# Optimization experiments

Hardware: AMD Instinct MI355X
Metric: run time of the kernel (lower is better)

Reference implementation:

```python
import jax, jax.numpy as jnp
import numpy as np

N, H, G = 500_000, 128, 50_000


def setup_inputs() -> dict:
    key = jax.random.key(0)
    k1, k2, k3, k4, k5, k6, k7 = jax.random.split(key, 7)
    x_src = jax.random.normal(k1, (N, H), dtype=jnp.float32)
    imputed_embs = jax.random.normal(k2, (G, H), dtype=jnp.float32)
    src_ids = jnp.sort(jax.random.randint(k3, (N,), 0, G, dtype=jnp.int32))
    s = 1.0 / np.sqrt(2 * H)
    W1 = jax.random.uniform(k4, (H, 2 * H), jnp.float32, -s, s)  # cat_linear1
    b1 = jax.random.uniform(k5, (H,), jnp.float32, -s, s)
    W2 = jax.random.uniform(k6, (H, 2 * H), jnp.float32, -s, s)  # cat_linear2
    b2 = jax.random.uniform(k7, (H,), jnp.float32, -s, s)
    return {"x_src": x_src, "imputed_embs": imputed_embs, "W1": W1, "b1": b1,
            "W2": W2, "b2": b2, "src_ids": src_ids}


def reference(x_src, imputed_embs, W1, b1, W2, b2, src_ids):
    n, h = x_src.shape
    g = imputed_embs.shape[0]
    # group index per row: boundaries where adjacent sorted src_ids differ
    boundary = jnp.concatenate([jnp.zeros((1,), jnp.int32),
                                (src_ids[1:] != src_ids[:-1]).astype(jnp.int32)])
    gid = jnp.cumsum(boundary)  # [N] group id (0..num_groups-1)
    # segment mean of x_src per group (parallel replacement of the python loop)
    seg_sum = jax.ops.segment_sum(x_src, gid, num_segments=g)
    counts = jax.ops.segment_sum(jnp.ones((n,), x_src.dtype), gid, num_segments=g)
    seg_mean = seg_sum / jnp.maximum(counts, 1.0)[:, None]
    # original loop never writes the mean for the LAST group (or unused rows):
    written = (jnp.arange(g) < gid[-1])[:, None]
    imp_second = jnp.where(written, seg_mean, imputed_embs)
    # x_out rows: [x_src_i, imputed_embs[group(i)]]
    x_cat = jnp.concatenate([x_src, imputed_embs[gid]], axis=1)      # [N, 2H]
    imp_cat = jnp.concatenate([imputed_embs, imp_second], axis=1)    # [G, 2H]
    x_out = x_cat @ W1.T + b1
    imputed_out = imp_cat @ W2.T + b2
    return (x_out, imputed_out)
```

## Files before the change

kernel.cpp:

```cpp
#include <hip/hip_runtime.h>

typedef __attribute__((ext_vector_type(8))) short short8;
typedef __attribute__((ext_vector_type(4))) float f32x4;

static __device__ __forceinline__ unsigned short f2bf(float f) {
    union { float f; unsigned int u; } v; v.f = f;
    unsigned int r = v.u + 0x7fffu + ((v.u >> 16) & 1u);
    return (unsigned short)(r >> 16);
}

static __device__ __forceinline__ short8 pack8(float4 a, float4 b) {
    short8 r;
    r[0] = (short)f2bf(a.x); r[1] = (short)f2bf(a.y);
    r[2] = (short)f2bf(a.z); r[3] = (short)f2bf(a.w);
    r[4] = (short)f2bf(b.x); r[5] = (short)f2bf(b.y);
    r[6] = (short)f2bf(b.z); r[7] = (short)f2bf(b.w);
    return r;
}

static __device__ __forceinline__ void dma16(const void* g, void* l) {
    __builtin_amdgcn_global_load_lds(
        (const __attribute__((address_space(1))) unsigned int*)g,
        (__attribute__((address_space(3))) unsigned int*)l, 16, 0, 0);
}

static __device__ __forceinline__ float4 lds_rd16(const float* buf, int boff, int sw) {
    return *(const float4*)((const char*)buf + (boff ^ sw));
}

__global__ void k_zero(uint4* p, int n16) {
    int i = blockIdx.x * blockDim.x + threadIdx.x;
    if (i < n16) p[i] = uint4{0u, 0u, 0u, 0u};
}

__global__ void k_convw(const float* __restrict__ W1, const float* __restrict__ W2,
                        unsigned short* W1af, unsigned short* W1bf,
                        unsigned short* W2af, unsigned short* W2bf) {
    int T = blockIdx.x * 256 + threadIdx.x;
    int mat = T >> 11;
    int rem = T & 2047;
    int f = rem >> 6, lane = rem & 63;
    int wc = f >> 4, t = (f >> 2) & 3, kk = f & 3;
    int p = lane & 15, q = lane >> 4;
    int row = wc * 64 + t * 16 + p;
    int col = (mat & 1) * 128 + kk * 32 + q * 8;
    const float* src = (mat < 2 ? W1 : W2) + row * 256 + col;
    unsigned short* dst = (mat == 0 ? W1af : mat == 1 ? W1bf : mat == 2 ? W2af : W2bf);
    short8 v;
#pragma unroll
    for (int j = 0; j < 8; ++j) v[j] = (short)f2bf(src[j]);
    *(short8*)&dst[(size_t)f * 512 + lane * 8] = v;
}

__global__ void k_mark(const int* __restrict__ ids, int* __restrict__ cum, int n) {
    int i = blockIdx.x * blockDim.x + threadIdx.x;
    if (i < n) cum[ids[i]] = 1;
}

__global__ __launch_bounds__(256) void k_scan1(int* __restrict__ cum, int* __restrict__ bsum, int G) {
    __shared__ int ws[4];
    int tid = threadIdx.x;
    int base = blockIdx.x * 1024 + tid * 4;
    int a0 = 0, a1 = 0, a2 = 0, a3 = 0;
    if (base + 0 < G) a0 = cum[base + 0];
    if (base + 1 < G) a1 = cum[base + 1];
    if (base + 2 < G) a2 = cum[base + 2];
    if (base + 3 < G) a3 = cum[base + 3];
    int s = a0 + a1 + a2 + a3;
    int lane = tid & 63;
    int v = s;
#pragma unroll
    for (int off = 1; off < 64; off <<= 1) {
        int u = __shfl_up(v, off, 64);
        if (lane >= off) v += u;
    }
    if (lane == 63) ws[tid >> 6] = v;
    __syncthreads();
    int wof = 0;
    for (int w = 0; w < (tid >> 6); ++w) wof += ws[w];
    int excl = wof + v - s;
    int r0 = excl + a0, r1 = r0 + a1, r2 = r1 + a2, r3 = r2 + a3;
    if (base + 0 < G) cum[base + 0] = r0;
    if (base + 1 < G) cum[base + 1] = r1;
    if (base + 2 < G) cum[base + 2] = r2;
    if (base + 3 < G) cum[base + 3] = r3;
    if (tid == 255) bsum[blockIdx.x] = excl + s;
}

__global__ void k_scan2(int* __restrict__ bsum, int nb) {
    int t = threadIdx.x;
    int v = (t < nb) ? bsum[t] : 0;
#pragma unroll
    for (int off = 1; off < 64; off <<= 1) {
        int u = __shfl_up(v, off, 64);
        if (t >= off) v += u;
    }
    if (t < nb) bsum[t] = v;
}

__global__ void k_gid(const int* __restrict__ ids, const int* __restrict__ cum,
                      const int* __restrict__ bsum, int* __restrict__ gid,
                      int* __restrict__ gstart, int* __restrict__ ngr, int n) {
    int i = blockIdx.x * blockDim.x + threadIdx.x;
    if (i >= n) return;
    int v = ids[i];
    int blk = v >> 10;
    int g = cum[v] + (blk ? bsum[blk - 1] : 0) - 1;
    gid[i] = g;
    if (i == 0 || ids[i - 1] != v) gstart[g] = i;
    if (i == n - 1) { gstart[g + 1] = n; *ngr = g + 1; }
}

__global__ __launch_bounds__(256, 2) void k_egemm(
    const float* __restrict__ emb, const unsigned short* __restrict__ Wf,
    const float* __restrict__ b1, float* __restrict__ E1, int G) {
    __shared__ __align__(16) float ebuf[16384];
    int tid = threadIdx.x, lane = tid & 63, wid = tid >> 6;
    int p = lane & 15, q = lane >> 4;
    int wr = wid >> 1, wc = wid & 1;
    int row0 = blockIdx.x * 128;

    short8 bfr[4][4];
#pragma unroll
    for (int t = 0; t < 4; ++t)
#pragma unroll
        for (int kk = 0; kk < 4; ++kk)
            bfr[t][kk] = *(const short8*)&Wf[(size_t)((wc * 4 + t) * 4 + kk) * 512 + lane * 8];
    float b1v[4];
#pragma unroll
    for (int t = 0; t < 4; ++t) b1v[t] = b1[wc * 64 + t * 16 + p];

    long long maxb = (long long)G * 512 - 16;
#pragma unroll
    for (int k = 0; k < 16; ++k) {
        int doff = k * 4096 + tid * 16;
        int r = doff >> 9;
        long long s = (long long)(row0 + r) * 512 + (long long)((doff & 511) ^ ((r & 7) << 4));
        s = s < maxb ? s : maxb;
        dma16((const char*)emb + s, (char*)ebuf + doff);
    }
    asm volatile("s_waitcnt vmcnt(0)" ::: "memory");
    __builtin_amdgcn_s_barrier();
    __builtin_amdgcn_sched_barrier(0);

    int sw = (p & 7) << 4;
#pragma unroll
    for (int tt = 0; tt < 4; ++tt) {
        int lr = wr * 64 + tt * 16 + p;
        short8 afr[4];
#pragma unroll
        for (int kk = 0; kk < 4; ++kk) {
            int boff = lr * 512 + kk * 128 + q * 32;
            float4 v0 = lds_rd16(ebuf, boff, sw);
            float4 v1 = lds_rd16(ebuf, boff + 16, sw);
            afr[kk] = pack8(v0, v1);
        }
        f32x4 acc[4];
#pragma unroll
        for (int t = 0; t < 4; ++t) acc[t] = f32x4{0.f, 0.f, 0.f, 0.f};
#pragma unroll
        for (int t = 0; t < 4; ++t)
#pragma unroll
            for (int kk = 0; kk < 4; ++kk)
                acc[t] = __builtin_amdgcn_mfma_f32_16x16x32_bf16(afr[kk], bfr[t][kk], acc[t], 0, 0, 0);
#pragma unroll
        for (int t = 0; t < 4; ++t) {
            int colb = wc * 64 + t * 16 + p;
#pragma unroll
            for (int rg = 0; rg < 4; ++rg) {
                int rr = row0 + wr * 64 + tt * 16 + q * 4 + rg;
                if (rr < G) E1[(size_t)rr * 128 + colb] = acc[t][rg] + b1v[t];
            }
        }
    }
}

__global__ __launch_bounds__(256, 2) void k_xgemm(
    const float* __restrict__ x, const unsigned short* __restrict__ Wf,
    const int* __restrict__ gid, const float* __restrict__ E1,
    const int* __restrict__ gstart, const int* __restrict__ ngr,
    float* __restrict__ out, unsigned short* __restrict__ imps,
    float* __restrict__ segsum, int N, int nwg) {
    __shared__ __align__(16) float xbuf[16384];
    int tid = threadIdx.x, lane = tid & 63, wid = tid >> 6;
    int p = lane & 15, q = lane >> 4;
    int wr = wid >> 1, wc = wid & 1;
    int orig = blockIdx.x;
    int qq = nwg >> 3, rr8 = nwg & 7;
    int xcd = orig & 7, idx = orig >> 3;
    int bid = (xcd < rr8 ? xcd * (qq + 1) : rr8 * (qq + 1) + (xcd - rr8) * qq) + idx;
    int row0 = bid * 128;

    short8 bfr[4][4];
#pragma unroll
    for (int t = 0; t < 4; ++t)
#pragma unroll
        for (int kk = 0; kk < 4; ++kk)
            bfr[t][kk] = *(const short8*)&Wf[(size_t)((wc * 4 + t) * 4 + kk) * 512 + lane * 8];

    int gt0 = gid[min(row0 + wr * 64 + 0 * 16 + p, N - 1)];
    int gt1 = gid[min(row0 + wr * 64 + 1 * 16 + p, N - 1)];
    int gt2 = gid[min(row0 + wr * 64 + 2 * 16 + p, N - 1)];
    int gt3 = gid[min(row0 + wr * 64 + 3 * 16 + p, N - 1)];

    long long maxb = (long long)N * 512 - 16;
#pragma unroll
    for (int k = 0; k < 16; ++k) {
        int doff = k * 4096 + tid * 16;
        int r = doff >> 9;
        long long s = (long long)(row0 + r) * 512 + (long long)((doff & 511) ^ ((r & 7) << 4));
        s = s < maxb ? s : maxb;
        dma16((const char*)x + s, (char*)xbuf + doff);
    }
    asm volatile("s_waitcnt vmcnt(0)" ::: "memory");
    __builtin_amdgcn_s_barrier();
    __builtin_amdgcn_sched_barrier(0);

    int sw = (p & 7) << 4;
#pragma unroll
    for (int tt = 0; tt < 4; ++tt) {
        int gt = (tt == 0) ? gt0 : (tt == 1) ? gt1 : (tt == 2) ? gt2 : gt3;
        int lr = wr * 64 + tt * 16 + p;
        short8 afr[4];
#pragma unroll
        for (int kk = 0; kk < 4; ++kk) {
            int boff = lr * 512 + kk * 128 + q * 32;
            float4 v0 = lds_rd16(xbuf, boff, sw);
            float4 v1 = lds_rd16(xbuf, boff + 16, sw);
            afr[kk] = pack8(v0, v1);
        }
        int g4[4];
#pragma unroll
        for (int rg = 0; rg < 4; ++rg) g4[rg] = __shfl(gt, q * 4 + rg);
        float ev[4][4];
#pragma unroll
        for (int t = 0; t < 4; ++t) {
            int colb = wc * 64 + t * 16 + p;
#pragma unroll
            for (int rg = 0; rg < 4; ++rg)
                ev[t][rg] = E1[(size_t)g4[rg] * 128 + colb];
        }
        f32x4 acc[4];
#pragma unroll
        for (int t = 0; t < 4; ++t) acc[t] = f32x4{0.f, 0.f, 0.f, 0.f};
#pragma unroll
        for (int t = 0; t < 4; ++t)
#pragma unroll
            for (int kk = 0; kk < 4; ++kk)
                acc[t] = __builtin_amdgcn_mfma_f32_16x16x32_bf16(afr[kk], bfr[t][kk], acc[t], 0, 0, 0);
#pragma unroll
        for (int t = 0; t < 4; ++t) {
            int colb = wc * 64 + t * 16 + p;
#pragma unroll
            for (int rg = 0; rg < 4; ++rg) {
                int rr = row0 + wr * 64 + tt * 16 + q * 4 + rg;
                if (rr < N) out[(size_t)rr * 128 + colb] = acc[t][rg] + ev[t][rg];
            }
        }
    }

    int c = tid & 127;
    int h = tid >> 7;
    int lo = row0 + h * 64;
    if (lo < N) {
        int hi = min(lo + 64, N);
        int ng = *ngr;
        int g = gid[lo];
        int rs = gstart[g];
        for (;;) {
            int re = gstart[g + 1];
            int a = rs > lo ? rs : lo;
            int b = re < hi ? re : hi;
            float s = 0.f;
            for (int r = a; r < b; ++r) {
                int lrr = r - row0;
                s += *(const float*)((const char*)xbuf + lrr * 512 + ((c * 4) ^ ((lrr & 7) << 4)));
            }
            bool contained = (rs >= lo) && (re <= hi);
            if (contained) {
                if (g < ng - 1)
                    imps[(size_t)g * 128 + c] = f2bf(s / (float)(re - rs));
            } else {
                atomicAdd(&segsum[(size_t)g * 128 + c], s);
            }
            if (re >= hi) break;
            rs = re; ++g;
        }
    }
}

__global__ __launch_bounds__(256) void k_fix(
    const float* __restrict__ segsum, const float* __restrict__ emb,
    const int* __restrict__ gstart, const int* __restrict__ ngr,
    unsigned short* __restrict__ imps, int G) {
    int g = blockIdx.x * 4 + (threadIdx.x >> 6);
    int lane = threadIdx.x & 63;
    if (g >= G) return;
    int ng = *ngr;
    float2 m;
    if (g < ng - 1) {
        int a = gstart[g], b = gstart[g + 1];
        if ((a >> 6) == ((b - 1) >> 6)) return;
        float inv = 1.0f / (float)(b - a);
        float2 s = *(const float2*)&segsum[(size_t)g * 128 + lane * 2];
        m.x = s.x * inv; m.y = s.y * inv;
    } else {
        m = *(const float2*)&emb[(size_t)g * 128 + lane * 2];
    }
    unsigned int pk = (unsigned int)f2bf(m.x) | ((unsigned int)f2bf(m.y) << 16);
    ((unsigned int*)imps)[(size_t)g * 64 + lane] = pk;
}

__global__ __launch_bounds__(256, 2) void k_igemm(
    const float* __restrict__ emb, const unsigned short* __restrict__ imps,
    const unsigned short* __restrict__ Waf, const unsigned short* __restrict__ Wbf,
    const float* __restrict__ b2, float* __restrict__ out2, int G) {
    __shared__ __align__(16) float ebuf[8192];
    __shared__ __align__(16) unsigned short ibuf[8192];
    int tid = threadIdx.x, lane = tid & 63, wid = tid >> 6;
    int p = lane & 15, q = lane >> 4;
    int wr = wid >> 1, wc = wid & 1;
    int row0 = blockIdx.x * 64;

    short8 bfrA[4][4], bfrB[4][4];
#pragma unroll
    for (int t = 0; t < 4; ++t)
#pragma unroll
        for (int kk = 0; kk < 4; ++kk) {
            bfrA[t][kk] = *(const short8*)&Waf[(size_t)((wc * 4 + t) * 4 + kk) * 512 + lane * 8];
            bfrB[t][kk] = *(const short8*)&Wbf[(size_t)((wc * 4 + t) * 4 + kk) * 512 + lane * 8];
        }
    float b2v[4];
#pragma unroll
    for (int t = 0; t < 4; ++t) b2v[t] = b2[wc * 64 + t * 16 + p];

    long long maxe = (long long)G * 512 - 16;
    long long maxi = (long long)G * 256 - 16;
#pragma unroll
    for (int k = 0; k < 8; ++k) {
        int doff = k * 4096 + tid * 16;
        int r = doff >> 9;
        long long s = (long long)(row0 + r) * 512 + (long long)((doff & 511) ^ ((r & 7) << 4));
        s = s < maxe ? s : maxe;
        dma16((const char*)emb + s, (char*)ebuf + doff);
    }
#pragma unroll
    for (int k = 0; k < 4; ++k) {
        int doff = k * 4096 + tid * 16;
        int r = doff >> 8;
        long long s = (long long)(row0 + r) * 256 + (long long)((doff & 255) ^ ((r & 7) << 4));
        s = s < maxi ? s : maxi;
        dma16((const char*)imps + s, (char*)ibuf + doff);
    }
    asm volatile("s_waitcnt vmcnt(0)" ::: "memory");
    __builtin_amdgcn_s_barrier();
    __builtin_amdgcn_sched_barrier(0);

    int sw = (p & 7) << 4;
#pragma unroll
    for (int tt = 0; tt < 2; ++tt) {
        int lr = wr * 32 + tt * 16 + p;
        short8 ae[4], ia[4];
#pragma unroll
        for (int kk = 0; kk < 4; ++kk) {
            int boff = lr * 512 + kk * 128 + q * 32;
            float4 v0 = lds_rd16(ebuf, boff, sw);
            float4 v1 = lds_rd16(ebuf, boff + 16, sw);
            ae[kk] = pack8(v0, v1);
            int boff2 = lr * 256 + ((kk * 64 + q * 16) ^ sw);
            ia[kk] = *(const short8*)((const char*)ibuf + boff2);
        }
        f32x4 acc[4];
#pragma unroll
        for (int t = 0; t < 4; ++t) acc[t] = f32x4{0.f, 0.f, 0.f, 0.f};
#pragma unroll
        for (int kk = 0; kk < 4; ++kk)
#pragma unroll
            for (int t = 0; t < 4; ++t) {
                acc[t] = __builtin_amdgcn_mfma_f32_16x16x32_bf16(ae[kk], bfrA[t][kk], acc[t], 0, 0, 0);
                acc[t] = __builtin_amdgcn_mfma_f32_16x16x32_bf16(ia[kk], bfrB[t][kk], acc[t], 0, 0, 0);
            }
#pragma unroll
        for (int t = 0; t < 4; ++t) {
            int colb = wc * 64 + t * 16 + p;
#pragma unroll
            for (int rg = 0; rg < 4; ++rg) {
                int rr = row0 + wr * 32 + tt * 16 + q * 4 + rg;
                if (rr < G) out2[(size_t)rr * 128 + colb] = acc[t][rg] + b2v[t];
            }
        }
    }
}

extern "C" void kernel_launch(void* const* d_in, const int* in_sizes, int n_in,
                              void* d_out, int out_size, void* d_ws, size_t ws_size,
                              hipStream_t stream) {
    const float* x   = (const float*)d_in[0];
    const float* emb = (const float*)d_in[1];
    const float* W1  = (const float*)d_in[2];
    const float* b1  = (const float*)d_in[3];
    const float* W2  = (const float*)d_in[4];
    const float* b2  = (const float*)d_in[5];
    const int*   ids = (const int*)d_in[6];
    const int H = 128;
    const int N = in_sizes[6];
    const int G = in_sizes[1] / H;

    float* out  = (float*)d_out;
    float* out2 = out + (size_t)N * H;
    float* E1   = out2;

    char* ws = (char*)d_ws;
    size_t off = 0;
    float* segsum = (float*)(ws + off); off += (size_t)G * H * 4;
    int*   cum    = (int*)(ws + off);   off += (size_t)G * 4;
    size_t zbytes = off;
    off = (off + 255) & ~(size_t)255;
    int* bsum   = (int*)(ws + off); off += 64 * 4;          off = (off + 255) & ~(size_t)255;
    int* gid    = (int*)(ws + off); off += (size_t)N * 4;   off = (off + 255) & ~(size_t)255;
    int* gstart = (int*)(ws + off); off += (size_t)(G + 1) * 4; off = (off + 255) & ~(size_t)255;
    int* ngr    = (int*)(ws + off); off += 256;
    unsigned short* W1af = (unsigned short*)(ws + off); off += (size_t)H * H * 2;
    unsigned short* W1bf = (unsigned short*)(ws + off); off += (size_t)H * H * 2;
    unsigned short* W2af = (unsigned short*)(ws + off); off += (size_t)H * H * 2;
    unsigned short* W2bf = (unsigned short*)(ws + off); off += (size_t)H * H * 2;
    unsigned short* imps = (unsigned short*)(ws + off); off += (size_t)G * H * 2;

    int n16 = (int)((zbytes + 15) / 16);
    int nb = (G + 1023) >> 10;
    int nwgX = (N + 127) >> 7;
    int nwgE = (G + 127) >> 7;
    int nwgI = (G + 63) >> 6;
    k_zero<<<(n16 + 255) / 256, 256, 0, stream>>>((uint4*)ws, n16);
    k_convw<<<32, 256, 0, stream>>>(W1, W2, W1af, W1bf, W2af, W2bf);
    k_mark<<<(N + 255) / 256, 256, 0, stream>>>(ids, cum, N);
    k_scan1<<<nb, 256, 0, stream>>>(cum, bsum, G);
    k_scan2<<<1, 64, 0, stream>>>(bsum, nb);
    k_gid<<<(N + 255) / 256, 256, 0, stream>>>(ids, cum, bsum, gid, gstart, ngr, N);
    k_egemm<<<nwgE, 256, 0, stream>>>(emb, W1bf, b1, E1, G);
    k_xgemm<<<nwgX, 256, 0, stream>>>(x, W1af, gid, E1, gstart, ngr, out, imps, segsum, N, nwgX);
    k_fix<<<(G + 3) / 4, 256, 0, stream>>>(segsum, emb, gstart, ngr, imps, G);
    k_igemm<<<nwgI, 256, 0, stream>>>(emb, imps, W2af, W2bf, b2, out2, G);
}
```

Measured before the change: 219.1 us.

## Hoist E1 gathers before MMA loop and stream segment sums via shared group ids

Moves all E1 gathers for the four row tiles ahead of the MFMA loop, so their latency overlaps with compute instead of stalling each tile's epilogue. Replaces the gstart-driven segment walk with a single streaming pass over the 64-row window. Group ids are staged in shared memory, and boundaries are detected from neighbouring gids plus the gids just before and after the window. This removes dependent global loads of gstart inside the reduction loop and batches LDS reads eight at a time. The trade-off is higher register pressure, since ev now holds 64 floats per thread, which could cut occupancy under launch_bounds(256,2).

```diff
diff --git a/kernel.cpp b/kernel.cpp
--- a/kernel.cpp
+++ b/kernel.cpp
@@ -178,10 +178,11 @@
 __global__ __launch_bounds__(256, 2) void k_xgemm(
     const float* __restrict__ x, const unsigned short* __restrict__ Wf,
     const int* __restrict__ gid, const float* __restrict__ E1,
-    const int* __restrict__ gstart, const int* __restrict__ ngr,
+    const int* __restrict__ ngr,
     float* __restrict__ out, unsigned short* __restrict__ imps,
     float* __restrict__ segsum, int N, int nwg) {
     __shared__ __align__(16) float xbuf[16384];
+    __shared__ int gids[128];
     int tid = threadIdx.x, lane = tid & 63, wid = tid >> 6;
     int p = lane & 15, q = lane >> 4;
     int wr = wid >> 1, wc = wid & 1;
@@ -198,10 +199,17 @@
         for (int kk = 0; kk < 4; ++kk)
             bfr[t][kk] = *(const short8*)&Wf[(size_t)((wc * 4 + t) * 4 + kk) * 512 + lane * 8];
 
-    int gt0 = gid[min(row0 + wr * 64 + 0 * 16 + p, N - 1)];
-    int gt1 = gid[min(row0 + wr * 64 + 1 * 16 + p, N - 1)];
-    int gt2 = gid[min(row0 + wr * 64 + 2 * 16 + p, N - 1)];
-    int gt3 = gid[min(row0 + wr * 64 + 3 * 16 + p, N - 1)];
+    int gt[4];
+#pragma unroll
+    for (int tt = 0; tt < 4; ++tt)
+        gt[tt] = gid[min(row0 + wr * 64 + tt * 16 + p, N - 1)];
+
+    int c = tid & 127, h = tid >> 7;
+    int lo = row0 + h * 64;
+    int hi = min(lo + 64, N);
+    int gbefore = -1, gafter = -1;
+    if (lo > 0 && lo < N) gbefore = gid[lo - 1];
+    if (hi < N) gafter = gid[hi];
 
     long long maxb = (long long)N * 512 - 16;
 #pragma unroll
@@ -212,14 +220,33 @@
         s = s < maxb ? s : maxb;
         dma16((const char*)x + s, (char*)xbuf + doff);
     }
-    asm volatile("s_waitcnt vmcnt(0)" ::: "memory");
+    if (wc == 0) {
+#pragma unroll
+        for (int tt = 0; tt < 4; ++tt)
+            gids[wr * 64 + tt * 16 + p] = gt[tt];
+    }
+    asm volatile("s_waitcnt vmcnt(0) lgkmcnt(0)" ::: "memory");
     __builtin_amdgcn_s_barrier();
     __builtin_amdgcn_sched_barrier(0);
 
+    float ev[4][4][4];
+#pragma unroll
+    for (int tt = 0; tt < 4; ++tt) {
+        int g4[4];
+#pragma unroll
+        for (int rg = 0; rg < 4; ++rg) g4[rg] = __shfl(gt[tt], q * 4 + rg);
+#pragma unroll
+        for (int t = 0; t < 4; ++t) {
+            int colb = wc * 64 + t * 16 + p;
+#pragma unroll
+            for (int rg = 0; rg < 4; ++rg)
+                ev[tt][t][rg] = E1[(size_t)g4[rg] * 128 + colb];
+        }
+    }
+
     int sw = (p & 7) << 4;
 #pragma unroll
     for (int tt = 0; tt < 4; ++tt) {
-        int gt = (tt == 0) ? gt0 : (tt == 1) ? gt1 : (tt == 2) ? gt2 : gt3;
         int lr = wr * 64 + tt * 16 + p;
         short8 afr[4];
 #pragma unroll
@@ -229,62 +256,63 @@
             float4 v1 = lds_rd16(xbuf, boff + 16, sw);
             afr[kk] = pack8(v0, v1);
         }
-        int g4[4];
-#pragma unroll
-        for (int rg = 0; rg < 4; ++rg) g4[rg] = __shfl(gt, q * 4 + rg);
-        float ev[4][4];
+        f32x4 acc[4];
+#pragma unroll
+        for (int t = 0; t < 4; ++t) acc[t] = f32x4{0.f, 0.f, 0.f, 0.f};
+#pragma unroll
+        for (int t = 0; t < 4; ++t)
+#pragma unroll
+            for (int kk = 0; kk < 4; ++kk)
+                acc[t] = __builtin_amdgcn_mfma_f32_16x16x32_bf16(afr[kk], bfr[t][kk], acc[t], 0, 0, 0);
 #pragma unroll
         for (int t = 0; t < 4; ++t) {
             int colb = wc * 64 + t * 16 + p;
 #pragma unroll
-            for (int rg = 0; rg < 4; ++rg)
-                ev[t][rg] = E1[(size_t)g4[rg] * 128 + colb];
-        }
-        f32x4 acc[4];
-#pragma unroll
-        for (int t = 0; t < 4; ++t) acc[t] = f32x4{0.f, 0.f, 0.f, 0.f};
-#pragma unroll
-        for (int t = 0; t < 4; ++t)
-#pragma unroll
-            for (int kk = 0; kk < 4; ++kk)
-                acc[t] = __builtin_amdgcn_mfma_f32_16x16x32_bf16(afr[kk], bfr[t][kk], acc[t], 0, 0, 0);
-#pragma unroll
-        for (int t = 0; t < 4; ++t) {
-            int colb = wc * 64 + t * 16 + p;
-#pragma unroll
             for (int rg = 0; rg < 4; ++rg) {
                 int rr = row0 + wr * 64 + tt * 16 + q * 4 + rg;
-                if (rr < N) out[(size_t)rr * 128 + colb] = acc[t][rg] + ev[t][rg];
-            }
-        }
-    }
-
-    int c = tid & 127;
-    int h = tid >> 7;
-    int lo = row0 + h * 64;
+                if (rr < N) out[(size_t)rr * 128 + colb] = acc[t][rg] + ev[tt][t][rg];
+            }
+        }
+    }
+
     if (lo < N) {
-        int hi = min(lo + 64, N);
+        int nwin = hi - lo;
+        int gbase = h * 64;
         int ng = *ngr;
-        int g = gid[lo];
-        int rs = gstart[g];
-        for (;;) {
-            int re = gstart[g + 1];
-            int a = rs > lo ? rs : lo;
-            int b = re < hi ? re : hi;
-            float s = 0.f;
-            for (int r = a; r < b; ++r) {
-                int lrr = r - row0;
-                s += *(const float*)((const char*)xbuf + lrr * 512 + ((c * 4) ^ ((lrr & 7) << 4)));
-            }
-            bool contained = (rs >= lo) && (re <= hi);
-            if (contained) {
-                if (g < ng - 1)
-                    imps[(size_t)g * 128 + c] = f2bf(s / (float)(re - rs));
-            } else {
-                atomicAdd(&segsum[(size_t)g * 128 + c], s);
-            }
-            if (re >= hi) break;
-            rs = re; ++g;
+        int gcur = gids[gbase];
+        bool open_left = (gcur == gbefore);
+        int rs = lo;
+        float s = 0.f;
+        for (int bb = 0; bb < nwin; bb += 8) {
+            float v[8];
+            int gn[8];
+#pragma unroll
+            for (int j = 0; j < 8; ++j) {
+                int rr = bb + j; rr = rr < nwin - 1 ? rr : nwin - 1;
+                int lrr = gbase + rr;
+                v[j] = *(const float*)((const char*)xbuf + lrr * 512 + ((c * 4) ^ ((lrr & 7) << 4)));
+                int rn = bb + j + 1; rn = rn < nwin - 1 ? rn : nwin - 1;
+                gn[j] = gids[gbase + rn];
+            }
+#pragma unroll
+            for (int j = 0; j < 8; ++j) {
+                int r = bb + j;
+                if (r < nwin) {
+                    s += v[j];
+                    bool at_end = (r + 1 >= nwin);
+                    int gnext = at_end ? gafter : gn[j];
+                    if (at_end || gnext != gcur) {
+                        bool open_right = at_end && (gafter == gcur);
+                        if (!open_left && !open_right) {
+                            if (gcur < ng - 1)
+                                imps[(size_t)gcur * 128 + c] = f2bf(s / (float)(lo + r + 1 - rs));
+                        } else {
+                            atomicAdd(&segsum[(size_t)gcur * 128 + c], s);
+                        }
+                        s = 0.f; rs = lo + r + 1; gcur = gnext; open_left = false;
+                    }
+                }
+            }
         }
     }
 }
@@ -438,7 +466,7 @@
     k_scan2<<<1, 64, 0, stream>>>(bsum, nb);
     k_gid<<<(N + 255) / 256, 256, 0, stream>>>(ids, cum, bsum, gid, gstart, ngr, N);
     k_egemm<<<nwgE, 256, 0, stream>>>(emb, W1bf, b1, E1, G);
-    k_xgemm<<<nwgX, 256, 0, stream>>>(x, W1af, gid, E1, gstart, ngr, out, imps, segsum, N, nwgX);
+    k_xgemm<<<nwgX, 256, 0, stream>>>(x, W1af, gid, E1, ngr, out, imps, segsum, N, nwgX);
     k_fix<<<(G + 3) / 4, 256, 0, stream>>>(segsum, emb, gstart, ngr, imps, G);
     k_igemm<<<nwgI, 256, 0, stream>>>(emb, imps, W2af, W2bf, b2, out2, G);
 }
```

Result: faster. 208.2 us (-5.0%).
